# Kernel optimization log

Hardware: AMD Instinct MI355X
Metric: run time of the kernel (lower is better)

The kernel has to match this reference:

```python
import jax, jax.numpy as jnp
import numpy as np

B, T, D = 2, 2048, 1024   # batch, seq_len, d_model
R, RS = 64, 16            # feature-mixing rank, DPLR sequence-mixing rank

_PARAM_SHAPES = [
    # LowRankFeatureMixing (qk gate path): q, m_gate, k projections (rank-R)
    ("qk_Wq1", (D, R)), ("qk_Wq2", (R, D)), ("qk_Wm1", (D, R)), ("qk_Wm2", (R, D)), ("qk_Wk1", (D, R)), ("qk_Wk2", (R, D)),
    # LowRankFeatureMixing (qk scale path, HyperGLU)
    ("qks_Wq1", (D, R)), ("qks_Wq2", (R, D)), ("qks_Wm1", (D, R)), ("qks_Wm2", (R, D)), ("qks_Wk1", (D, R)), ("qks_Wk2", (R, D)),
    # LowRankFeatureMixing (vo / readout path): v, m_vo projections + static W_O
    ("vo_Wv1", (D, R)), ("vo_Wv2", (R, D)), ("vo_Wm1", (D, R)), ("vo_Wm2", (R, D)), ("vo_Wo", (D, D)),
    # DPLRSequenceMixing 1 (gate): diag + low-rank factors generated from x
    ("sm1_Wd", (D, 1)), ("sm1_Wa", (D, RS)), ("sm1_Wb", (D, RS)),
    # DPLRSequenceMixing 1 (scale, HyperGLU)
    ("sm1s_Wd", (D, 1)), ("sm1s_Wa", (D, RS)), ("sm1s_Wb", (D, RS)),
    # DPLRSequenceMixing 2 (readout)
    ("sm2_Wd", (D, 1)), ("sm2_Wa", (D, RS)), ("sm2_Wb", (D, RS)),
]


def setup_inputs() -> dict:
    key = jax.random.key(0)
    keys = jax.random.split(key, len(_PARAM_SHAPES) + 1)
    inp = {"x": jax.random.normal(keys[0], (B, T, D), dtype=jnp.float32)}
    for k, (name, shape) in zip(keys[1:], _PARAM_SHAPES):
        scale = shape[0] ** -0.5
        inp[name] = jax.random.normal(k, shape, dtype=jnp.float32) * scale
    return inp


def _lowrank(x, Wa, Wb):
    # x: [b,t,d] -> [b,t,d] via rank-R factorization
    return (x @ Wa) @ Wb


def _dplr_mix(x, z, Wd, Wa, Wb):
    """Apply R(x) = diag(d(x)) + A(x) B(x)^T on the kv axis of z [b,tq,tkv]."""
    d = x @ Wd                       # [b,t,1] data-dependent diagonal
    A = x @ Wa                       # [b,t,rs]
    Bm = x @ Wb                      # [b,t,rs]
    zB = jnp.einsum('bij,bjr->bir', z, Bm)          # [b,t,rs]
    return z * jnp.swapaxes(d, 1, 2) + jnp.einsum('bir,bjr->bij', zB, A)


def reference(x, qk_Wq1, qk_Wq2, qk_Wm1, qk_Wm2, qk_Wk1, qk_Wk2,
              qks_Wq1, qks_Wq2, qks_Wm1, qks_Wm2, qks_Wk1, qks_Wk2,
              vo_Wv1, vo_Wv2, vo_Wm1, vo_Wm2, vo_Wo,
              sm1_Wd, sm1_Wa, sm1_Wb, sm1s_Wd, sm1s_Wa, sm1s_Wb,
              sm2_Wd, sm2_Wa, sm2_Wb):
    # Feature mixing (gate, scale, vo paths)
    q  = _lowrank(x, qk_Wq1, qk_Wq2);   mg  = _lowrank(x, qk_Wm1, qk_Wm2);   k  = _lowrank(x, qk_Wk1, qk_Wk2)
    qs = _lowrank(x, qks_Wq1, qks_Wq2); mgs = _lowrank(x, qks_Wm1, qks_Wm2); ks = _lowrank(x, qks_Wk1, qks_Wk2)
    v  = _lowrank(x, vo_Wv1, vo_Wv2);   mvo = _lowrank(x, vo_Wm1, vo_Wm2)

    # QK-like scores, [b,t,t]
    z  = jnp.einsum('bid,bjd->bij', q * mg, k)
    zs = jnp.einsum('bid,bjd->bij', qs * mgs, ks)

    # First DPLR sequence mixing + L2-norm over kv axis (gate branch)
    h_mix = _dplr_mix(x, z, sm1_Wd, sm1_Wa, sm1_Wb)
    h_mix = h_mix / (jnp.linalg.norm(h_mix, axis=-1, keepdims=True) + 1e-8)
    # Scale branch (HyperGLU)
    h_scale = _dplr_mix(x, zs, sm1s_Wd, sm1s_Wa, sm1s_Wb)
    h = jax.nn.softplus(h_scale) * jax.nn.relu(h_mix)

    # Second DPLR mixing -> readout weights, then context + output projection
    readout = _dplr_mix(x, h, sm2_Wd, sm2_Wa, sm2_Wb)      # [b,t,t]
    context = jnp.einsum('bij,bjd->bid', readout, v)        # [b,t,d]
    return (context * mvo) @ vo_Wo.T
```

## Files before the change

### kernel.cpp

```cpp
#include <hip/hip_runtime.h>
#include <math.h>

#define BB 2
#define TT 2048
#define DD 1024
#define RS 16
#define MT (BB*TT)
#define GLD 640
#define KAUG 1056

typedef __attribute__((ext_vector_type(8))) short s16x8;
typedef __attribute__((ext_vector_type(4))) float f32x4;

__device__ __forceinline__ short f2bf(float f) {
    union { float f; unsigned u; } v; v.f = f;
    unsigned r = (v.u + 0x7fffu + ((v.u >> 16) & 1u)) >> 16;
    return (short)r;
}
__device__ __forceinline__ float bf2f(short s) {
    union { unsigned u; float f; } v; v.u = ((unsigned)(unsigned short)s) << 16;
    return v.f;
}

__device__ __forceinline__ void gload16(const void* g, void* l) {
    __builtin_amdgcn_global_load_lds((const __attribute__((address_space(1))) void*)g,
                                     (__attribute__((address_space(3))) void*)l, 16, 0, 0);
}

__device__ __forceinline__ void xcd_swz(int& bx, int& by, int& bz)
{
    const int gx = gridDim.x, gy = gridDim.y;
    const int n = gx * gy * (int)gridDim.z;
    int flat = (bz * gy + by) * gx + bx;
    const int cpx = n >> 3;
    flat = (flat & 7) * cpx + (flat >> 3);
    bx = flat % gx; by = (flat / gx) % gy; bz = flat / (gx * gy);
}

template<int DEPTH>
__device__ __forceinline__ void gemm_core128p(const short* __restrict__ A,
                                              const short* __restrict__ Bt,
                                              int K, int lda, int ldb,
                                              int bi, int bj, short* smem,
                                              f32x4 (&acc)[4][2])
{
    const int tid = threadIdx.x;
    const int wv = tid >> 6, lane = tid & 63;
    const int wr = (wv >> 2) * 64, wc = (wv & 3) * 32;

#pragma unroll
    for (int m = 0; m < 4; ++m)
#pragma unroll
        for (int n = 0; n < 2; ++n) acc[m][n] = (f32x4){0.f, 0.f, 0.f, 0.f};

    const int srow = wv * 16 + (lane >> 2);
    const int sg   = ((lane & 3) ^ ((srow >> 1) & 3)) * 8;
    const int frow = lane & 15;
    const int gidx = lane >> 4;
    const int koff = (gidx ^ ((frow >> 1) & 3)) * 8;

    const int nt = K >> 5;
    const long arow = (long)(bi + srow) * lda + sg;
    const long brow = (long)(bj + srow) * ldb + sg;

    auto stage = [&](int t, int q) {
        short* As = smem + q * 8192;
        short* Bs = As + 4096;
        const int k0 = t << 5;
        gload16(A + arow + k0, As + wv*512);
        gload16(Bt + brow + k0, Bs + wv*512);
    };

    stage(0, 0);
    if (nt > 1) stage(1, 1);
    if (DEPTH == 3) { if (nt > 2) stage(2, 2); }

    int q = 0;
    for (int t = 0; t < nt; ++t) {
        const int rem = nt - 1 - t;
        if (DEPTH == 3 && rem >= 2) asm volatile("s_waitcnt vmcnt(4)" ::: "memory");
        else if (rem >= 1)          asm volatile("s_waitcnt vmcnt(2)" ::: "memory");
        else                        asm volatile("s_waitcnt vmcnt(0)" ::: "memory");
        __builtin_amdgcn_s_barrier();

        const short* As = smem + q * 8192;
        const short* Bs = As + 4096;
        s16x8 af[4], bfr[2];
#pragma unroll
        for (int m = 0; m < 4; ++m)
            af[m] = *(const s16x8*)&As[(wr + m*16 + frow) * 32 + koff];
#pragma unroll
        for (int n = 0; n < 2; ++n)
            bfr[n] = *(const s16x8*)&Bs[(wc + n*16 + frow) * 32 + koff];
        asm volatile("s_waitcnt lgkmcnt(0)" ::: "memory");
        __builtin_amdgcn_sched_barrier(0);
        __builtin_amdgcn_s_barrier();

        if (t + DEPTH < nt) stage(t + DEPTH, q);

#pragma unroll
        for (int m = 0; m < 4; ++m)
#pragma unroll
            for (int n = 0; n < 2; ++n)
                acc[m][n] = __builtin_amdgcn_mfma_f32_16x16x32_bf16(af[m], bfr[n], acc[m][n], 0, 0, 0);
        q = (q == DEPTH - 1) ? 0 : q + 1;
    }
}

__device__ __forceinline__ void gemm_core128p4(const short* __restrict__ A,
                                               const short* __restrict__ Bt,
                                               int K, int lda, int ldb,
                                               int bi, int bj, short* smem,
                                               f32x4 (&acc)[4][4])
{
    const int tid = threadIdx.x;
    const int wv = tid >> 6, lane = tid & 63;
    const int wr = (wv >> 1) * 64, wc = (wv & 1) * 64;

#pragma unroll
    for (int m = 0; m < 4; ++m)
#pragma unroll
        for (int n = 0; n < 4; ++n) acc[m][n] = (f32x4){0.f, 0.f, 0.f, 0.f};

    const int srow = wv * 16 + (lane >> 2);
    const int sg   = ((lane & 3) ^ ((srow >> 1) & 3)) * 8;
    const int frow = lane & 15;
    const int gidx = lane >> 4;
    const int koff = (gidx ^ ((frow >> 1) & 3)) * 8;

    const int nt = K >> 5;
    const long arow = (long)(bi + srow) * lda + sg;
    const long brow = (long)(bj + srow) * ldb + sg;

    auto stage = [&](int t, int q) {
        short* As = smem + q * 8192;
        short* Bs = As + 4096;
        const int k0 = t << 5;
#pragma unroll
        for (int p = 0; p < 2; ++p) {
            gload16(A + arow + (long)p * 64 * lda + k0, As + p*2048 + wv*512);
            gload16(Bt + brow + (long)p * 64 * ldb + k0, Bs + p*2048 + wv*512);
        }
    };

    stage(0, 0);
    if (nt > 1) stage(1, 1);

    int q = 0;
    for (int t = 0; t < nt; ++t) {
        const int rem = nt - 1 - t;
        if (rem >= 1) asm volatile("s_waitcnt vmcnt(4)" ::: "memory");
        else          asm volatile("s_waitcnt vmcnt(0)" ::: "memory");
        __builtin_amdgcn_s_barrier();

        const short* As = smem + q * 8192;
        const short* Bs = As + 4096;
        s16x8 af[4], bfr[4];
#pragma unroll
        for (int m = 0; m < 4; ++m)
            af[m] = *(const s16x8*)&As[(wr + m*16 + frow) * 32 + koff];
#pragma unroll
        for (int n = 0; n < 4; ++n)
            bfr[n] = *(const s16x8*)&Bs[(wc + n*16 + frow) * 32 + koff];
        asm volatile("s_waitcnt lgkmcnt(0)" ::: "memory");
        __builtin_amdgcn_sched_barrier(0);
        __builtin_amdgcn_s_barrier();

        if (t + 2 < nt) stage(t + 2, q);

#pragma unroll
        for (int m = 0; m < 4; ++m)
#pragma unroll
            for (int n = 0; n < 4; ++n)
                acc[m][n] = __builtin_amdgcn_mfma_f32_16x16x32_bf16(af[m], bfr[n], acc[m][n], 0, 0, 0);
        q ^= 1;
    }
}

template<int STORE>
__global__ __launch_bounds__(512)
void gemm_nt(const short* __restrict__ A, const short* __restrict__ Bt,
             void* __restrict__ Cv, int K, int lda, int ldb, int ldc,
             long sA, long sB, long sC)
{
    int bx = blockIdx.x, by = blockIdx.y, bz = blockIdx.z;
    xcd_swz(bx, by, bz);
    const short* Ab = A  + (long)bz * sA;
    const short* Bb = Bt + (long)bz * sB;
    const int bi = by * 128, bj = bx * 128;
    __shared__ __align__(16) short smem[16384];
    f32x4 acc[4][2];
    gemm_core128p<2>(Ab, Bb, K, lda, ldb, bi, bj, smem, acc);

    const int lane = threadIdx.x & 63, wv = threadIdx.x >> 6;
    const int wr = (wv >> 2) * 64, wc = (wv & 3) * 32;
    const int col0 = lane & 15, row0 = (lane >> 4) * 4;
#pragma unroll
    for (int m = 0; m < 4; ++m)
#pragma unroll
        for (int n = 0; n < 2; ++n)
#pragma unroll
            for (int r = 0; r < 4; ++r) {
                int i = bi + wr + m*16 + row0 + r;
                int j = bj + wc + n*16 + col0;
                if (STORE == 0)
                    ((float*)Cv + (long)bz * sC)[(long)i * ldc + j] = acc[m][n][r];
                else
                    ((short*)Cv + (long)bz * sC)[(long)i * ldc + j] = f2bf(acc[m][n][r]);
            }
}

__global__ __launch_bounds__(512)
void gemm_s1(const short* __restrict__ xb, const short* __restrict__ WcatT,
             short* __restrict__ Gb512,
             float* __restrict__ d1, float* __restrict__ d1s, float* __restrict__ d2,
             float* __restrict__ B1T, float* __restrict__ B1sT, float* __restrict__ A2T,
             short* __restrict__ B2T,
             short* __restrict__ QGaug, short* __restrict__ QSGaug,
             short* __restrict__ KBaug, short* __restrict__ KSBaug)
{
    int bx = blockIdx.x, by = blockIdx.y, bz = blockIdx.z;
    xcd_swz(bx, by, bz);
    const int bi = by * 128, bj = bx * 128;
    __shared__ __align__(16) short smem[16384];
    f32x4 acc[4][2];
    gemm_core128p<2>(xb, WcatT, DD, DD, DD, bi, bj, smem, acc);

    const int lane = threadIdx.x & 63, wv = threadIdx.x >> 6;
    const int wr = (wv >> 2) * 64, wc = (wv & 3) * 32;
    const int col0 = lane & 15, row0 = (lane >> 4) * 4;
#pragma unroll
    for (int m = 0; m < 4; ++m)
#pragma unroll
        for (int n = 0; n < 2; ++n)
#pragma unroll
            for (int r = 0; r < 4; ++r) {
                int i = bi + wr + m*16 + row0 + r;
                int j = bj + wc + n*16 + col0;
                float val = acc[m][n][r];
                if (j < 512) {
                    Gb512[(long)i * 512 + j] = f2bf(val);
                } else if (j == 512) {
                    d1[i] = val;
                    for (int q = 0; q < RS; ++q) {
                        QGaug [(long)i * KAUG + 1040 + q] = 0;
                        QSGaug[(long)i * KAUG + 1040 + q] = 0;
                        KBaug [(long)i * KAUG + 1040 + q] = 0;
                        KSBaug[(long)i * KAUG + 1040 + q] = 0;
                    }
                } else if (j < 529) {
                    KBaug[(long)i * KAUG + 1024 + (j - 513)] = f2bf(val);
                } else if (j < 545) {
                    B1T[(long)(j - 529) * MT + i] = val;
                } else if (j == 545) {
                    d1s[i] = val;
                } else if (j < 562) {
                    KSBaug[(long)i * KAUG + 1024 + (j - 546)] = f2bf(val);
                } else if (j < 578) {
                    B1sT[(long)(j - 562) * MT + i] = val;
                } else if (j == 578) {
                    d2[i] = val;
                } else if (j < 595) {
                    A2T[(long)(j - 579) * MT + i] = val;
                } else if (j < 611) {
                    B2T[(long)(j - 595) * MT + i] = f2bf(val);
                }
            }
}

__global__ __launch_bounds__(256)
void e_kernel(const short* __restrict__ Gb512, const float* __restrict__ BT0,
              float* __restrict__ E)
{
    const int tc = blockIdx.x, b = blockIdx.y, kind = blockIdx.z;
    const int col0 = (kind == 0) ? 128 : (kind == 1) ? 320 : 384;
    const float* BT = BT0 + (size_t)kind * RS * MT;
    const int c = threadIdx.x & 63, rg = threadIdx.x >> 6;
    float acc[4] = {0.f, 0.f, 0.f, 0.f};
    const int t0 = tc * (TT / 16);
#pragma unroll 2
    for (int tt = 0; tt < TT / 16; ++tt) {
        const long gi = (long)b * TT + t0 + tt;
        float g = bf2f(Gb512[gi * 512 + col0 + c]);
#pragma unroll
        for (int q = 0; q < 4; ++q)
            acc[q] = fmaf(g, BT[(long)(rg * 4 + q) * MT + gi], acc[q]);
    }
#pragma unroll
    for (int q = 0; q < 4; ++q)
        atomicAdd(&E[(((long)kind * BB + b) * 64 + c) * RS + rg * 4 + q], acc[q]);
}

__global__ __launch_bounds__(256)
void c1w_kernel(const short* __restrict__ W2, const float* __restrict__ E,
                float* __restrict__ C1, float* __restrict__ A2tV)
{
    const int d0 = blockIdx.x * 64, kind = blockIdx.y, b = blockIdx.z;
    const int s = (kind == 0) ? 2 : (kind == 1) ? 5 : 6;
    __shared__ float El[64][RS];
    {
        const float* Eb = E + ((long)kind * BB + b) * 64 * RS;
        int q = threadIdx.x;
#pragma unroll
        for (int k = 0; k < 4; ++k) ((float*)El)[q + 256 * k] = Eb[q + 256 * k];
    }
    __syncthreads();
    const int dl = threadIdx.x & 63, rg = threadIdx.x >> 6;
    const int d = d0 + dl;
    const short* wrow = W2 + ((long)s * DD + d) * 64;
    float acc[4] = {0.f, 0.f, 0.f, 0.f};
#pragma unroll
    for (int c8 = 0; c8 < 8; ++c8) {
        s16x8 wv = *(const s16x8*)&wrow[c8 * 8];
#pragma unroll
        for (int u = 0; u < 8; ++u) {
            float w = bf2f(wv[u]);
#pragma unroll
            for (int q = 0; q < 4; ++q)
                acc[q] = fmaf(w, El[c8 * 8 + u][rg * 4 + q], acc[q]);
        }
    }
    if (kind < 2) {
        float* dst = C1 + (size_t)kind * BB * DD * RS;
#pragma unroll
        for (int q = 0; q < 4; ++q)
            dst[((long)b * DD + d) * RS + rg * 4 + q] = acc[q];
    } else {
#pragma unroll
        for (int q = 0; q < 4; ++q)
            A2tV[((long)b * RS + rg * 4 + q) * DD + d] = acc[q];
    }
}

__global__ __launch_bounds__(256)
void hmhs_kernel(const short* __restrict__ QGaug, const short* __restrict__ QSGaug,
                 const short* __restrict__ KBaug, const short* __restrict__ KSBaug,
                 short* __restrict__ P, float* __restrict__ rowsum)
{
    int bx = blockIdx.x, by = blockIdx.y, bz = blockIdx.z;
    xcd_swz(bx, by, bz);
    const int b = bz;
    const int bi = by * 128, bj = bx * 128;
    __shared__ __align__(16) short smem[16384];
    f32x4 acc[4][4], acc2[4][4];
    gemm_core128p4(QGaug  + (long)b * TT * KAUG, KBaug  + (long)b * TT * KAUG,
                   KAUG, KAUG, KAUG, bi, bj, smem, acc);
    gemm_core128p4(QSGaug + (long)b * TT * KAUG, KSBaug + (long)b * TT * KAUG,
                   KAUG, KAUG, KAUG, bi, bj, smem, acc2);

    const int lane = threadIdx.x & 63, wv = threadIdx.x >> 6;
    const int wr = (wv >> 1) * 64, wc = (wv & 1) * 64;
    const int col0 = lane & 15, row0 = (lane >> 4) * 4;
    short* Pb = P + (long)b * TT * TT;

    float ss[4][4];
#pragma unroll
    for (int m = 0; m < 4; ++m)
#pragma unroll
        for (int r = 0; r < 4; ++r) ss[m][r] = 0.f;

#pragma unroll
    for (int m = 0; m < 4; ++m)
#pragma unroll
        for (int n = 0; n < 4; ++n)
#pragma unroll
            for (int r = 0; r < 4; ++r) {
                int i = bi + wr + m*16 + row0 + r;
                int j = bj + wc + n*16 + col0;
                float hmv = acc[m][n][r];
                float sv  = acc2[m][n][r];
                float sp  = fmaxf(sv, 0.f) + __logf(1.f + __expf(-fabsf(sv)));
                Pb[(long)i * TT + j] = f2bf(sp * fmaxf(hmv, 0.f));
                ss[m][r] = fmaf(hmv, hmv, ss[m][r]);
            }

#pragma unroll
    for (int m = 0; m < 4; ++m)
#pragma unroll
        for (int r = 0; r < 4; ++r) {
            float v = ss[m][r];
            v += __shfl_xor(v, 1, 64);
            v += __shfl_xor(v, 2, 64);
            v += __shfl_xor(v, 4, 64);
            v += __shfl_xor(v, 8, 64);
            if (col0 == 0)
                atomicAdd(&rowsum[(long)b * TT + bi + wr + m*16 + row0 + r], v);
        }
}

__global__ __launch_bounds__(256)
void finish_kernel(const short* __restrict__ P, const short* __restrict__ B2T,
                   const float* __restrict__ rowsum, float* __restrict__ hB)
{
    const int i = blockIdx.x, b = blockIdx.y, tid = threadIdx.x;
    const long gi = (long)b * TT + i;
    const float inv = 1.f / (sqrtf(rowsum[gi]) + 1e-8f);
    const short* Pr = P + ((long)b * TT + i) * TT;
    const long tb = (long)b * TT;
    const int j0 = tid * 8;

    float hb[RS];
#pragma unroll
    for (int r = 0; r < RS; ++r) hb[r] = 0.f;

    s16x8 pv = *(const s16x8*)&Pr[j0];
    float pf[8];
#pragma unroll
    for (int q = 0; q < 8; ++q) pf[q] = bf2f(pv[q]);
#pragma unroll
    for (int r = 0; r < RS; ++r) {
        s16x8 bv = *(const s16x8*)&B2T[(long)r * MT + tb + j0];
#pragma unroll
        for (int q = 0; q < 8; ++q) hb[r] = fmaf(pf[q], bf2f(bv[q]), hb[r]);
    }
#pragma unroll
    for (int r = 0; r < RS; ++r)
#pragma unroll
        for (int off = 32; off; off >>= 1) hb[r] += __shfl_down(hb[r], off, 64);
    __shared__ float red[4][RS];
    if ((tid & 63) == 0)
#pragma unroll
        for (int r = 0; r < RS; ++r) red[tid >> 6][r] = hb[r];
    __syncthreads();
    if (tid < RS)
        hB[gi * RS + tid] = (red[0][tid] + red[1][tid] + red[2][tid] + red[3][tid]) * inv;
}

struct S2S { int mode, sa, sb; short* outS; const float* rs; };
struct S2A { S2S sl[6]; };

__global__ __launch_bounds__(512)
void stage2_kernel(const short* __restrict__ Gb, const short* __restrict__ W2,
                   S2A args)
{
    int bx = blockIdx.x, by = blockIdx.y, bz = blockIdx.z;
    xcd_swz(bx, by, bz);
    const S2S sl = args.sl[bz];
    const int bi = by * 128, bj = bx * 128;
    __shared__ __align__(16) short smem[16384];
    f32x4 acc[4][2];
    gemm_core128p<2>(Gb + sl.sa * 64, W2 + (long)sl.sa * DD * 64, 64, 512, 64, bi, bj, smem, acc);
    f32x4 acc2[4][2];
    if (sl.mode == 0)
        gemm_core128p<2>(Gb + sl.sb * 64, W2 + (long)sl.sb * DD * 64, 64, 512, 64, bi, bj, smem, acc2);

    const int lane = threadIdx.x & 63, wv = threadIdx.x >> 6;
    const int wr = (wv >> 2) * 64, wc = (wv & 3) * 32;
    const int col0 = lane & 15, row0 = (lane >> 4) * 4;
#pragma unroll
    for (int m = 0; m < 4; ++m)
#pragma unroll
        for (int n = 0; n < 2; ++n)
#pragma unroll
            for (int r = 0; r < 4; ++r) {
                int i = bi + wr + m*16 + row0 + r;
                int j = bj + wc + n*16 + col0;
                float val = acc[m][n][r];
                if (sl.mode == 0) {
                    sl.outS[(long)i * KAUG + j] = f2bf(val * acc2[m][n][r]);
                } else if (sl.mode == 1) {
                    sl.outS[(long)i * KAUG + j] = f2bf(val * sl.rs[i]);
                } else {
                    sl.outS[(long)i * DD + j] = f2bf(val);
                }
            }
}

__global__ __launch_bounds__(512)
void ctx_kernel(const short* __restrict__ P, const short* __restrict__ VDT,
                const short* __restrict__ mvo, const float* __restrict__ hB,
                const float* __restrict__ A2tV, const float* __restrict__ rowsum,
                short* __restrict__ cm)
{
    int bx = blockIdx.x, by = blockIdx.y, bz = blockIdx.z;
    xcd_swz(bx, by, bz);
    const int b = bz;
    const int bi = by * 128, bj = bx * 128;
    __shared__ __align__(16) short smem[24576];
    f32x4 acc[4][2];
    gemm_core128p<3>(P + (long)b * TT * TT, VDT + (long)b * DD * TT, TT, TT, TT, bi, bj, smem, acc);

    const int lane = threadIdx.x & 63, wv = threadIdx.x >> 6;
    const int wr = (wv >> 2) * 64, wc = (wv & 3) * 32;
    const int col0 = lane & 15, row0 = (lane >> 4) * 4;
    const float* a2 = A2tV + (long)b * RS * DD;

#pragma unroll
    for (int m = 0; m < 4; ++m)
#pragma unroll
        for (int r = 0; r < 4; ++r) {
            long gi = (long)b * TT + bi + wr + m*16 + row0 + r;
            float iv = 1.f / (sqrtf(rowsum[gi]) + 1e-8f);
#pragma unroll
            for (int n = 0; n < 2; ++n) acc[m][n][r] *= iv;
        }

#pragma unroll
    for (int r16 = 0; r16 < RS; ++r16) {
        float a2v[2];
#pragma unroll
        for (int n = 0; n < 2; ++n)
            a2v[n] = a2[(long)r16 * DD + bj + wc + n*16 + col0];
#pragma unroll
        for (int m = 0; m < 4; ++m)
#pragma unroll
            for (int r = 0; r < 4; ++r) {
                long gi = (long)b * TT + bi + wr + m*16 + row0 + r;
                float hb = hB[gi * RS + r16];
#pragma unroll
                for (int n = 0; n < 2; ++n)
                    acc[m][n][r] = fmaf(hb, a2v[n], acc[m][n][r]);
            }
    }
#pragma unroll
    for (int m = 0; m < 4; ++m)
#pragma unroll
        for (int n = 0; n < 2; ++n)
#pragma unroll
            for (int r = 0; r < 4; ++r) {
                long gi = (long)b * TT + bi + wr + m*16 + row0 + r;
                int j = bj + wc + n*16 + col0;
                cm[gi * DD + j] = f2bf(acc[m][n][r] * bf2f(mvo[gi * DD + j]));
            }
}

struct ConcatArgs { const float* p[17]; int col0[17]; int wid[17]; };

__global__ __launch_bounds__(256)
void concat_w1_kernel(ConcatArgs a, short* __restrict__ WcatT,
                      float* __restrict__ zp, int zn)
{
    const int q = blockIdx.x * 256 + threadIdx.x;
    if (q < zn) zp[q] = 0.f;
    const int n = blockIdx.x;
    int s = -1, c = 0;
    for (int i = 0; i < 17; ++i)
        if (n >= a.col0[i] && n < a.col0[i] + a.wid[i]) { s = i; c = n - a.col0[i]; }
    for (int k = threadIdx.x; k < DD; k += 256)
        WcatT[(long)n * DD + k] = (s < 0) ? (short)0 : f2bf(a.p[s][(long)k * a.wid[s] + c]);
}

struct Ptrs8 { const float* p[8]; };

__global__ __launch_bounds__(256)
void concat_w2_kernel(Ptrs8 a, short* __restrict__ W2catT)
{
    const int s = blockIdx.y, n0 = blockIdx.x * 64;
    const int tx = threadIdx.x & 63, ty = threadIdx.x >> 6;
    __shared__ float t[64][65];
    const float* W2 = a.p[s];
    for (int kk = ty; kk < 64; kk += 4) t[kk][tx] = W2[(long)kk * DD + n0 + tx];
    __syncthreads();
    for (int n = ty; n < 64; n += 4)
        W2catT[((long)s * DD + n0 + n) * 64 + tx] = f2bf(t[tx][n]);
}

__global__ __launch_bounds__(256)
void f2bf_vec_kernel(const float* __restrict__ in, short* __restrict__ o, long n4)
{
    long i = (long)blockIdx.x * 256 + threadIdx.x;
    if (i < n4) {
        float4 v = ((const float4*)in)[i];
        short4 r; r.x = f2bf(v.x); r.y = f2bf(v.y); r.z = f2bf(v.z); r.w = f2bf(v.w);
        ((short4*)o)[i] = r;
    }
}

__global__ __launch_bounds__(256)
void zb_kernel(short* __restrict__ aug0, const float* __restrict__ C10)
{
    const int gi = blockIdx.x, path = blockIdx.y, b = gi >> 11, tid = threadIdx.x;
    short* aug = aug0 + (size_t)path * MT * KAUG;
    const float* c1 = C10 + (size_t)path * BB * DD * RS + (long)b * DD * RS;
    const short* qrow = aug + (long)gi * KAUG;
    float acc[RS];
#pragma unroll
    for (int r = 0; r < RS; ++r) acc[r] = 0.f;
#pragma unroll
    for (int c = 0; c < 4; ++c) {
        int d = tid + 256 * c;
        float q = bf2f(qrow[d]);
        const float* cr = c1 + (long)d * RS;
#pragma unroll
        for (int r = 0; r < RS; ++r) acc[r] = fmaf(q, cr[r], acc[r]);
    }
#pragma unroll
    for (int r = 0; r < RS; ++r)
#pragma unroll
        for (int off = 32; off; off >>= 1) acc[r] += __shfl_down(acc[r], off, 64);
    __shared__ float red[4][RS];
    if ((tid & 63) == 0)
#pragma unroll
        for (int r = 0; r < RS; ++r) red[tid >> 6][r] = acc[r];
    __syncthreads();
    if (tid < RS)
        aug[(long)gi * KAUG + 1024 + tid] =
            f2bf(red[0][tid] + red[1][tid] + red[2][tid] + red[3][tid]);
}

__global__ __launch_bounds__(256)
void vdt_kernel(const short* __restrict__ v, const float* __restrict__ d2,
                short* __restrict__ o)
{
    const int t0 = blockIdx.x * 32, d0 = blockIdx.y * 32, b = blockIdx.z;
    const int tx = threadIdx.x & 31, ty = threadIdx.x >> 5;
    __shared__ float tile[32][33];
    for (int s = 0; s < 32; s += 8) {
        int t = t0 + ty + s;
        tile[ty + s][tx] = bf2f(v[((long)b * TT + t) * DD + d0 + tx]) * d2[(long)b * TT + t];
    }
    __syncthreads();
    for (int s = 0; s < 32; s += 8) {
        int d = d0 + ty + s;
        o[((long)b * DD + d) * TT + t0 + tx] = f2bf(tile[tx][ty + s]);
    }
}

extern "C" void kernel_launch(void* const* d_in, const int* in_sizes, int n_in,
                              void* d_out, int out_size, void* d_ws, size_t ws_size,
                              hipStream_t stream)
{
    (void)in_sizes; (void)n_in; (void)out_size; (void)ws_size;
    const float* x = (const float*)d_in[0];
    const float* W[27];
    for (int i = 1; i < 27; ++i) W[i] = (const float*)d_in[i];
    float* out = (float*)d_out;

    char* ws = (char*)d_ws;
    size_t off = 0;
    auto alloc = [&](size_t bytes) -> void* {
        void* p = ws + off; off += (bytes + 255) & ~(size_t)255; return p;
    };
    short* xb     = (short*)alloc((size_t)MT * DD * 2);
    short* WcatT  = (short*)alloc((size_t)GLD * DD * 2);
    short* W2catT = (short*)alloc((size_t)8 * DD * 64 * 2);
    short* Gb512  = (short*)alloc((size_t)MT * 512 * 2);
    short* Wob    = (short*)alloc((size_t)DD * DD * 2);
    short* S1b    = (short*)alloc((size_t)MT * DD * 2);
    short* VB     = (short*)alloc((size_t)MT * DD * 2);
    short* QGaug  = (short*)alloc((size_t)MT * KAUG * 2);
    short* QSGaug = (short*)alloc((size_t)MT * KAUG * 2);
    short* KBaug  = (short*)alloc((size_t)MT * KAUG * 2);
    short* KSBaug = (short*)alloc((size_t)MT * KAUG * 2);
    short* CM     = (short*)alloc((size_t)MT * DD * 2);
    short* P      = (short*)alloc((size_t)BB * TT * TT * 2);
    float* d1   = (float*)alloc((size_t)MT * 4);
    float* d1s  = (float*)alloc((size_t)MT * 4);
    float* d2   = (float*)alloc((size_t)MT * 4);
    float* B1T  = (float*)alloc((size_t)RS * MT * 4);
    float* B1sT = (float*)alloc((size_t)RS * MT * 4);
    float* A2T  = (float*)alloc((size_t)RS * MT * 4);
    short* B2T  = (short*)alloc((size_t)RS * MT * 2);
    float* C1   = (float*)alloc((size_t)BB * DD * RS * 4);
    float* C1s  = (float*)alloc((size_t)BB * DD * RS * 4);
    float* A2tV = (float*)alloc((size_t)BB * RS * DD * 4);
    float* rowsum = (float*)alloc((size_t)MT * 4);
    float* E    = (float*)alloc((size_t)3 * BB * 64 * RS * 4);
    float* hB   = (float*)alloc((size_t)MT * RS * 4);

    short* VDT = xb;
    short* cm  = CM;

    const long n4 = (long)MT * DD / 4;
    const int ZN = MT + 3 * BB * 64 * RS;

    f2bf_vec_kernel<<<n4 / 256, 256, 0, stream>>>(x, xb, n4);
    ConcatArgs ca;
    {
        const int w1idx[8] = {1, 3, 5, 7, 9, 11, 13, 15};
        for (int s = 0; s < 8; ++s) { ca.p[s] = W[w1idx[s]]; ca.col0[s] = s * 64; ca.wid[s] = 64; }
        const int didx[9] = {18, 19, 20, 21, 22, 23, 24, 25, 26};
        const int dcol[9] = {512, 513, 529, 545, 546, 562, 578, 579, 595};
        const int dwid[9] = {1, 16, 16, 1, 16, 16, 1, 16, 16};
        for (int s = 0; s < 9; ++s) { ca.p[8 + s] = W[didx[s]]; ca.col0[8 + s] = dcol[s]; ca.wid[8 + s] = dwid[s]; }
    }
    concat_w1_kernel<<<GLD, 256, 0, stream>>>(ca, WcatT, rowsum, ZN);
    Ptrs8 p8;
    {
        const int w2idx[8] = {2, 4, 6, 8, 10, 12, 14, 16};
        for (int s = 0; s < 8; ++s) p8.p[s] = W[w2idx[s]];
    }
    concat_w2_kernel<<<dim3(DD / 64, 8), 256, 0, stream>>>(p8, W2catT);
    f2bf_vec_kernel<<<((long)DD * DD / 4) / 256, 256, 0, stream>>>(W[17], Wob, (long)DD * DD / 4);

    gemm_s1<<<dim3(GLD / 128, MT / 128, 1), 512, 0, stream>>>(
        xb, WcatT, Gb512, d1, d1s, d2, B1T, B1sT, A2T, B2T,
        QGaug, QSGaug, KBaug, KSBaug);

    e_kernel<<<dim3(16, BB, 3), 256, 0, stream>>>(Gb512, B1T, E);
    c1w_kernel<<<dim3(DD / 64, 3, BB), 256, 0, stream>>>(W2catT, E, C1, A2tV);

    S2A a;
    a.sl[0] = {0, 0, 1, QGaug,  nullptr};
    a.sl[1] = {0, 3, 4, QSGaug, nullptr};
    a.sl[2] = {1, 2, 0, KBaug,  d1};
    a.sl[3] = {1, 5, 0, KSBaug, d1s};
    a.sl[4] = {3, 6, 0, VB,     nullptr};
    a.sl[5] = {3, 7, 0, S1b,    nullptr};
    stage2_kernel<<<dim3(DD / 128, MT / 128, 6), 512, 0, stream>>>(Gb512, W2catT, a);

    vdt_kernel<<<dim3(TT / 32, DD / 32, BB), 256, 0, stream>>>(VB, d2, VDT);

    zb_kernel<<<dim3(MT, 2), 256, 0, stream>>>(QGaug, C1);

    hmhs_kernel<<<dim3(TT / 128, TT / 128, BB), 256, 0, stream>>>(
        QGaug, QSGaug, KBaug, KSBaug, P, rowsum);

    finish_kernel<<<dim3(TT, BB), 256, 0, stream>>>(P, B2T, rowsum, hB);

    ctx_kernel<<<dim3(DD / 128, TT / 128, BB), 512, 0, stream>>>(
        P, VDT, S1b, hB, A2tV, rowsum, cm);

    gemm_nt<0><<<dim3(DD / 128, MT / 128, 1), 512, 0, stream>>>(
        cm, Wob, out, DD, DD, DD, DD, 0, 0, 0);
}
```

Measured before the change: 263.2 us.

## Fuse h·B2 projection into hmhs epilogue and drop finish kernel

The separate finish kernel, which re-read the P matrix to compute the unnormalized h·B2 rank-16 projection, is removed. The hmhs kernel epilogue now computes these partial products from its fp32 register tile and accumulates them into hB with atomics. ctx_kernel adds the low-rank term before applying the row-norm inverse, so normalization stays correct. This saves a full read pass over P and one launch, but adds many more atomics and shuffle reductions to the hmhs epilogue and relies on hB being zeroed (ZN is extended to cover it).

```diff
diff --git a/kernel.cpp b/kernel.cpp
--- a/kernel.cpp
+++ b/kernel.cpp
@@ -335,7 +335,9 @@
 __global__ __launch_bounds__(256)
 void hmhs_kernel(const short* __restrict__ QGaug, const short* __restrict__ QSGaug,
                  const short* __restrict__ KBaug, const short* __restrict__ KSBaug,
-                 short* __restrict__ P, float* __restrict__ rowsum)
+                 const short* __restrict__ B2T,
+                 short* __restrict__ P, float* __restrict__ rowsum,
+                 float* __restrict__ hBraw)
 {
     int bx = blockIdx.x, by = blockIdx.y, bz = blockIdx.z;
     xcd_swz(bx, by, bz);
@@ -352,6 +354,7 @@
     const int wr = (wv >> 1) * 64, wc = (wv & 1) * 64;
     const int col0 = lane & 15, row0 = (lane >> 4) * 4;
     short* Pb = P + (long)b * TT * TT;
+    const long tb = (long)b * TT;
 
     float ss[4][4];
 #pragma unroll
@@ -370,8 +373,10 @@
                 float hmv = acc[m][n][r];
                 float sv  = acc2[m][n][r];
                 float sp  = fmaxf(sv, 0.f) + __logf(1.f + __expf(-fabsf(sv)));
-                Pb[(long)i * TT + j] = f2bf(sp * fmaxf(hmv, 0.f));
+                float hv  = sp * fmaxf(hmv, 0.f);
+                Pb[(long)i * TT + j] = f2bf(hv);
                 ss[m][r] = fmaf(hmv, hmv, ss[m][r]);
+                acc[m][n][r] = hv;
             }
 
 #pragma unroll
@@ -384,46 +389,30 @@
             v += __shfl_xor(v, 4, 64);
             v += __shfl_xor(v, 8, 64);
             if (col0 == 0)
-                atomicAdd(&rowsum[(long)b * TT + bi + wr + m*16 + row0 + r], v);
+                atomicAdd(&rowsum[tb + bi + wr + m*16 + row0 + r], v);
         }
-}
-
-__global__ __launch_bounds__(256)
-void finish_kernel(const short* __restrict__ P, const short* __restrict__ B2T,
-                   const float* __restrict__ rowsum, float* __restrict__ hB)
-{
-    const int i = blockIdx.x, b = blockIdx.y, tid = threadIdx.x;
-    const long gi = (long)b * TT + i;
-    const float inv = 1.f / (sqrtf(rowsum[gi]) + 1e-8f);
-    const short* Pr = P + ((long)b * TT + i) * TT;
-    const long tb = (long)b * TT;
-    const int j0 = tid * 8;
-
-    float hb[RS];
-#pragma unroll
-    for (int r = 0; r < RS; ++r) hb[r] = 0.f;
-
-    s16x8 pv = *(const s16x8*)&Pr[j0];
-    float pf[8];
-#pragma unroll
-    for (int q = 0; q < 8; ++q) pf[q] = bf2f(pv[q]);
-#pragma unroll
-    for (int r = 0; r < RS; ++r) {
-        s16x8 bv = *(const s16x8*)&B2T[(long)r * MT + tb + j0];
-#pragma unroll
-        for (int q = 0; q < 8; ++q) hb[r] = fmaf(pf[q], bf2f(bv[q]), hb[r]);
-    }
-#pragma unroll
-    for (int r = 0; r < RS; ++r)
-#pragma unroll
-        for (int off = 32; off; off >>= 1) hb[r] += __shfl_down(hb[r], off, 64);
-    __shared__ float red[4][RS];
-    if ((tid & 63) == 0)
-#pragma unroll
-        for (int r = 0; r < RS; ++r) red[tid >> 6][r] = hb[r];
-    __syncthreads();
-    if (tid < RS)
-        hB[gi * RS + tid] = (red[0][tid] + red[1][tid] + red[2][tid] + red[3][tid]) * inv;
+
+#pragma unroll 4
+    for (int r16 = 0; r16 < RS; ++r16) {
+        const short* br = B2T + (long)r16 * MT + tb + bj + wc;
+        float b2[4];
+#pragma unroll
+        for (int n = 0; n < 4; ++n) b2[n] = bf2f(br[n*16 + col0]);
+#pragma unroll
+        for (int m = 0; m < 4; ++m)
+#pragma unroll
+            for (int r = 0; r < 4; ++r) {
+                float v = 0.f;
+#pragma unroll
+                for (int n = 0; n < 4; ++n) v = fmaf(acc[m][n][r], b2[n], v);
+                v += __shfl_xor(v, 1, 64);
+                v += __shfl_xor(v, 2, 64);
+                v += __shfl_xor(v, 4, 64);
+                v += __shfl_xor(v, 8, 64);
+                if (col0 == 0)
+                    atomicAdd(&hBraw[(tb + bi + wr + m*16 + row0 + r) * RS + r16], v);
+            }
+    }
 }
 
 struct S2S { int mode, sa, sb; short* outS; const float* rs; };
@@ -468,7 +457,7 @@
 
 __global__ __launch_bounds__(512)
 void ctx_kernel(const short* __restrict__ P, const short* __restrict__ VDT,
-                const short* __restrict__ mvo, const float* __restrict__ hB,
+                const short* __restrict__ mvo, const float* __restrict__ hBraw,
                 const float* __restrict__ A2tV, const float* __restrict__ rowsum,
                 short* __restrict__ cm)
 {
@@ -486,42 +475,34 @@
     const float* a2 = A2tV + (long)b * RS * DD;
 
 #pragma unroll
+    for (int r16 = 0; r16 < RS; ++r16) {
+        float a2v[2];
+#pragma unroll
+        for (int n = 0; n < 2; ++n)
+            a2v[n] = a2[(long)r16 * DD + bj + wc + n*16 + col0];
+#pragma unroll
+        for (int m = 0; m < 4; ++m)
+#pragma unroll
+            for (int r = 0; r < 4; ++r) {
+                long gi = (long)b * TT + bi + wr + m*16 + row0 + r;
+                float hb = hBraw[gi * RS + r16];
+#pragma unroll
+                for (int n = 0; n < 2; ++n)
+                    acc[m][n][r] = fmaf(hb, a2v[n], acc[m][n][r]);
+            }
+    }
+#pragma unroll
     for (int m = 0; m < 4; ++m)
 #pragma unroll
         for (int r = 0; r < 4; ++r) {
             long gi = (long)b * TT + bi + wr + m*16 + row0 + r;
             float iv = 1.f / (sqrtf(rowsum[gi]) + 1e-8f);
 #pragma unroll
-            for (int n = 0; n < 2; ++n) acc[m][n][r] *= iv;
+            for (int n = 0; n < 2; ++n) {
+                int j = bj + wc + n*16 + col0;
+                cm[gi * DD + j] = f2bf(acc[m][n][r] * iv * bf2f(mvo[gi * DD + j]));
+            }
         }
-
-#pragma unroll
-    for (int r16 = 0; r16 < RS; ++r16) {
-        float a2v[2];
-#pragma unroll
-        for (int n = 0; n < 2; ++n)
-            a2v[n] = a2[(long)r16 * DD + bj + wc + n*16 + col0];
-#pragma unroll
-        for (int m = 0; m < 4; ++m)
-#pragma unroll
-            for (int r = 0; r < 4; ++r) {
-                long gi = (long)b * TT + bi + wr + m*16 + row0 + r;
-                float hb = hB[gi * RS + r16];
-#pragma unroll
-                for (int n = 0; n < 2; ++n)
-                    acc[m][n][r] = fmaf(hb, a2v[n], acc[m][n][r]);
-            }
-    }
-#pragma unroll
-    for (int m = 0; m < 4; ++m)
-#pragma unroll
-        for (int n = 0; n < 2; ++n)
-#pragma unroll
-            for (int r = 0; r < 4; ++r) {
-                long gi = (long)b * TT + bi + wr + m*16 + row0 + r;
-                int j = bj + wc + n*16 + col0;
-                cm[gi * DD + j] = f2bf(acc[m][n][r] * bf2f(mvo[gi * DD + j]));
-            }
 }
 
 struct ConcatArgs { const float* p[17]; int col0[17]; int wid[17]; };
@@ -662,7 +643,7 @@
     short* cm  = CM;
 
     const long n4 = (long)MT * DD / 4;
-    const int ZN = MT + 3 * BB * 64 * RS;
+    const int ZN = MT + 3 * BB * 64 * RS + MT * RS;
 
     f2bf_vec_kernel<<<n4 / 256, 256, 0, stream>>>(x, xb, n4);
     ConcatArgs ca;
@@ -704,9 +685,7 @@
     zb_kernel<<<dim3(MT, 2), 256, 0, stream>>>(QGaug, C1);
 
     hmhs_kernel<<<dim3(TT / 128, TT / 128, BB), 256, 0, stream>>>(
-        QGaug, QSGaug, KBaug, KSBaug, P, rowsum);
-
-    finish_kernel<<<dim3(TT, BB), 256, 0, stream>>>(P, B2T, rowsum, hB);
+        QGaug, QSGaug, KBaug, KSBaug, B2T, P, rowsum, hB);
 
     ctx_kernel<<<dim3(DD / 128, TT / 128, BB), 512, 0, stream>>>(
         P, VDT, S1b, hB, A2tV, rowsum, cm);
```

Measured after the change: 352.3 us. 33.8% more time.
